# Optimization experiments

Measured on AMD Instinct MI355X. Metric: run time of the kernel, lower is better.

Reference implementation:

```python
import jax, jax.numpy as jnp
import numpy as np

B, N, D, H = 4, 2048, 256, 8
DH = D // H

def setup_inputs() -> dict:
    key = jax.random.key(0)
    ks = jax.random.split(key, 7)
    s = 1.0 / np.sqrt(DH)
    return {
        "sequences": jax.random.normal(ks[0], (B, N, D), dtype=jnp.float32),
        "Wq": jax.random.uniform(ks[1], (H, DH, DH), jnp.float32, -s, s),
        "bq": jax.random.uniform(ks[2], (H, DH), jnp.float32, -s, s),
        "Wk": jax.random.uniform(ks[3], (H, DH, DH), jnp.float32, -s, s),
        "bk": jax.random.uniform(ks[4], (H, DH), jnp.float32, -s, s),
        "Wv": jax.random.uniform(ks[5], (H, DH, DH), jnp.float32, -s, s),
        "bv": jax.random.uniform(ks[6], (H, DH), jnp.float32, -s, s),
    }

def reference(sequences, Wq, bq, Wk, bk, Wv, bv):
    # sequences: [B, N, D] -> [B, N, H, DH] (head h sees columns h*DH:(h+1)*DH)
    x = sequences.reshape(B, N, H, DH)
    # per-head Linear: y = x @ W.T + b
    q = jnp.einsum("bnhd,hed->bnhe", x, Wq) + bq
    k = jnp.einsum("bnhd,hed->bnhe", x, Wk) + bk
    v = jnp.einsum("bnhd,hed->bnhe", x, Wv) + bv
    scores = jnp.einsum("bnhe,bmhe->bhnm", q, k) / jnp.sqrt(jnp.float32(DH))
    attn = jax.nn.softmax(scores, axis=-1)  # [B, H, N, N]
    out = jnp.einsum("bhnm,bmhe->bnhe", attn, v)
    # hstack of per-head results == concat over last dim == reshape
    return out.reshape(B, N, D)
```

## Files before the change

kernel.cpp:

```cpp
#include <hip/hip_runtime.h>
#include <hip/hip_bf16.h>

typedef __bf16 bf16;
typedef __bf16 bf16x8 __attribute__((ext_vector_type(8)));
typedef __bf16 bf16x4 __attribute__((ext_vector_type(4)));
typedef float  f32x4  __attribute__((ext_vector_type(4)));

#define B_  4
#define N_  2048
#define D_  256
#define H_  8
#define DH_ 32
#define QKV_ELEMS (B_*H_*N_*DH_)

#define QSC    (0.17677669529663687f * 1.4426950408889634f)
#define NBIAS  (-17.312340490667562f)

#if __has_builtin(__builtin_amdgcn_exp2f)
__device__ inline float exp2_hw(float x) { return __builtin_amdgcn_exp2f(x); }
#else
__device__ inline float exp2_hw(float x) {
    float r; asm volatile("v_exp_f32 %0, %1" : "=v"(r) : "v"(x)); return r;
}
#endif

__device__ inline bf16x8 ldcvt8(const float* __restrict__ p) {
    f32x4 a = *(const f32x4*)p;
    f32x4 b = *(const f32x4*)(p + 4);
    bf16x8 r;
    r[0] = (bf16)a[0]; r[1] = (bf16)a[1]; r[2] = (bf16)a[2]; r[3] = (bf16)a[3];
    r[4] = (bf16)b[0]; r[5] = (bf16)b[1]; r[6] = (bf16)b[2]; r[7] = (bf16)b[3];
    return r;
}

__global__ __launch_bounds__(256, 4) void qkv_proj_kernel(
    const float* __restrict__ x,
    const float* __restrict__ Wq, const float* __restrict__ bq,
    const float* __restrict__ Wk, const float* __restrict__ bk,
    const float* __restrict__ Wv, const float* __restrict__ bv,
    bf16* __restrict__ Qg, bf16* __restrict__ Kg, bf16* __restrict__ Vg)
{
    const int nt = blockIdx.x & 31, bh = blockIdx.x >> 5;
    const int h  = bh & (H_-1),    b  = bh >> 3;
    const int wave = threadIdx.x >> 6, lane = threadIdx.x & 63;
    const int l16 = lane & 15, q4 = lane >> 4;
    const int n0 = nt*64 + wave*16;

    bf16x8 xf = ldcvt8(x + ((size_t)(b*N_ + n0 + l16))*D_ + h*DH_ + q4*8);
    f32x4 z = {0.f,0.f,0.f,0.f};

    #pragma unroll
    for (int half = 0; half < 2; ++half) {
        {
            bf16x8 wqf = ldcvt8(Wq + (h*DH_ + half*16 + l16)*DH_ + q4*8);
            bf16x8 wkf = ldcvt8(Wk + (h*DH_ + half*16 + l16)*DH_ + q4*8);
            f32x4 dq = __builtin_amdgcn_mfma_f32_16x16x32_bf16(wqf, xf, z, 0, 0, 0);
            f32x4 dk = __builtin_amdgcn_mfma_f32_16x16x32_bf16(wkf, xf, z, 0, 0, 0);
            f32x4 bq4 = *(const f32x4*)(bq + h*DH_ + half*16 + q4*4);
            f32x4 bk4 = *(const f32x4*)(bk + h*DH_ + half*16 + q4*4);
            bf16x4 pq, pk;
            #pragma unroll
            for (int r = 0; r < 4; ++r) {
                pq[r] = (bf16)((dq[r] + bq4[r]) * QSC);
                pk[r] = (bf16)(dk[r] + bk4[r]);
            }
            const size_t row = ((size_t)bh*N_ + n0 + l16)*DH_ + half*16 + q4*4;
            *(bf16x4*)(Qg + row) = pq;
            *(bf16x4*)(Kg + row) = pk;
        }
        {
            bf16x8 wvf = ldcvt8(Wv + (h*DH_ + half*16 + l16)*DH_ + q4*8);
            f32x4 dv = __builtin_amdgcn_mfma_f32_16x16x32_bf16(xf, wvf, z, 0, 0, 0);
            const float bb = bv[h*DH_ + half*16 + l16];
            bf16x4 pv;
            #pragma unroll
            for (int r = 0; r < 4; ++r) pv[r] = (bf16)(dv[r] + bb);
            const int e = half*16 + l16;
            const size_t idx = ((size_t)bh << 16) + ((size_t)(n0 >> 5) << 10)
                             + (e << 5) + (q4 << 3) + (((n0 >> 4) & 1) << 2);
            *(bf16x4*)(Vg + idx) = pv;
        }
    }
}

__global__ __launch_bounds__(256, 2) void attn_kernel(
    const bf16* __restrict__ Qg, const bf16* __restrict__ Kg,
    const bf16* __restrict__ Vg, float* __restrict__ out)
{
    const int qt = blockIdx.x & 15;
    const int bh = blockIdx.x >> 4;
    const int h  = bh & (H_-1), b = bh >> 3;
    const int lane = threadIdx.x & 63;
    const int wave = threadIdx.x >> 6;
    const int l16 = lane & 15, q4 = lane >> 4;

    const bf16* Kb = Kg + (size_t)bh*N_*DH_;
    const bf16* Vb = Vg + ((size_t)bh << 16);
    const int qrow0 = qt*128 + wave*32;

    bf16x8 qb0 = *(const bf16x8*)(Qg + ((size_t)bh*N_ + qrow0 + l16)*DH_ + q4*8);
    bf16x8 qb1 = *(const bf16x8*)(Qg + ((size_t)bh*N_ + qrow0 + 16 + l16)*DH_ + q4*8);

    bf16x8 ones;
    #pragma unroll
    for (int j = 0; j < 8; ++j) ones[j] = (bf16)1.0f;

    f32x4 ot[2][2];
    f32x4 osum[2];
    #pragma unroll
    for (int i = 0; i < 2; ++i) {
        ot[i][0] = (f32x4){0,0,0,0}; ot[i][1] = (f32x4){0,0,0,0};
        osum[i]  = (f32x4){0,0,0,0};
    }

    bf16x8 kf[8], vf[8];
    #pragma unroll
    for (int kc = 0; kc < 8; ++kc)
        kf[kc] = *(const bf16x8*)(Kb + (size_t)(kc*16 + l16)*DH_ + q4*8);
    #pragma unroll
    for (int i = 0; i < 8; ++i)
        vf[i] = *(const bf16x8*)(Vb + (size_t)(i >> 1)*1024 + ((i & 1)*16 + l16)*32 + q4*8);

    const f32x4 zb = {NBIAS, NBIAS, NBIAS, NBIAS};

    for (int kt = 0; kt < 16; ++kt) {
        f32x4 st[8][2];
        #pragma unroll
        for (int kc = 0; kc < 8; ++kc) {
            st[kc][0] = __builtin_amdgcn_mfma_f32_16x16x32_bf16(kf[kc], qb0, zb, 0, 0, 0);
            st[kc][1] = __builtin_amdgcn_mfma_f32_16x16x32_bf16(kf[kc], qb1, zb, 0, 0, 0);
        }

        const int nkt = (kt + 1) & 15;
        const bf16* Kn = Kb + (size_t)nkt*128*DH_;
        #pragma unroll
        for (int kc = 0; kc < 8; ++kc)
            kf[kc] = *(const bf16x8*)(Kn + (size_t)(kc*16 + l16)*DH_ + q4*8);

        bf16x8 pb[4][2];
        #pragma unroll
        for (int kc = 0; kc < 8; ++kc)
            #pragma unroll
            for (int qh = 0; qh < 2; ++qh)
                #pragma unroll
                for (int r = 0; r < 4; ++r)
                    pb[kc >> 1][qh][(kc & 1)*4 + r] = (bf16)exp2_hw(st[kc][qh][r]);

        #pragma unroll
        for (int kk = 0; kk < 4; ++kk) {
            #pragma unroll
            for (int dhh = 0; dhh < 2; ++dhh) {
                ot[dhh][0] = __builtin_amdgcn_mfma_f32_16x16x32_bf16(vf[kk*2 + dhh], pb[kk][0], ot[dhh][0], 0, 0, 0);
                ot[dhh][1] = __builtin_amdgcn_mfma_f32_16x16x32_bf16(vf[kk*2 + dhh], pb[kk][1], ot[dhh][1], 0, 0, 0);
            }
            osum[0] = __builtin_amdgcn_mfma_f32_16x16x32_bf16(ones, pb[kk][0], osum[0], 0, 0, 0);
            osum[1] = __builtin_amdgcn_mfma_f32_16x16x32_bf16(ones, pb[kk][1], osum[1], 0, 0, 0);
        }

        const bf16* Vn = Vb + (size_t)nkt*128*DH_;
        #pragma unroll
        for (int i = 0; i < 8; ++i)
            vf[i] = *(const bf16x8*)(Vn + (size_t)(i >> 1)*1024 + ((i & 1)*16 + l16)*32 + q4*8);
    }

    #pragma unroll
    for (int qh = 0; qh < 2; ++qh) {
        const float inv = 1.0f / osum[qh][0];
        #pragma unroll
        for (int dhh = 0; dhh < 2; ++dhh) {
            f32x4 o;
            #pragma unroll
            for (int r = 0; r < 4; ++r) o[r] = ot[dhh][qh][r] * inv;
            *(f32x4*)(out + ((size_t)b*N_ + qrow0 + qh*16 + l16)*D_
                          + h*DH_ + dhh*16 + q4*4) = o;
        }
    }
}

extern "C" void kernel_launch(void* const* d_in, const int* in_sizes, int n_in,
                              void* d_out, int out_size, void* d_ws, size_t ws_size,
                              hipStream_t stream)
{
    const float* x  = (const float*)d_in[0];
    const float* Wq = (const float*)d_in[1];
    const float* bq = (const float*)d_in[2];
    const float* Wk = (const float*)d_in[3];
    const float* bk = (const float*)d_in[4];
    const float* Wv = (const float*)d_in[5];
    const float* bv = (const float*)d_in[6];
    float* out = (float*)d_out;

    bf16* Qg = (bf16*)d_ws;
    bf16* Kg = Qg + QKV_ELEMS;
    bf16* Vg = Kg + QKV_ELEMS;

    qkv_proj_kernel<<<dim3(B_*H_*(N_/64)), dim3(256), 0, stream>>>(
        x, Wq, bq, Wk, bk, Wv, bv, Qg, Kg, Vg);
    attn_kernel<<<dim3(B_*H_*(N_/128)), dim3(256), 0, stream>>>(Qg, Kg, Vg, out);
}
```

Before: 116.5 us.

## Halve attention query tile per wave and loop projection blocks over four row tiles

The attention kernel now gives each wave 16 query rows instead of 32 and launches twice as many blocks with occupancy hint 4. This lowers register pressure and raises parallelism, but every K/V tile is re-read by twice as many waves. The V fragments are now loaded inside the current iteration instead of prefetched, so load latency may be exposed. The projection kernel loads weights and biases once per block, loops over four 64-row tiles, and uses a quarter of the blocks.

```diff
diff --git a/kernel.cpp b/kernel.cpp
--- a/kernel.cpp
+++ b/kernel.cpp
@@ -40,41 +40,45 @@
     const float* __restrict__ Wv, const float* __restrict__ bv,
     bf16* __restrict__ Qg, bf16* __restrict__ Kg, bf16* __restrict__ Vg)
 {
-    const int nt = blockIdx.x & 31, bh = blockIdx.x >> 5;
-    const int h  = bh & (H_-1),    b  = bh >> 3;
+    const int nt8 = blockIdx.x & 7, bh = blockIdx.x >> 3;
+    const int h   = bh & (H_-1),   b  = bh >> 3;
     const int wave = threadIdx.x >> 6, lane = threadIdx.x & 63;
     const int l16 = lane & 15, q4 = lane >> 4;
-    const int n0 = nt*64 + wave*16;
 
-    bf16x8 xf = ldcvt8(x + ((size_t)(b*N_ + n0 + l16))*D_ + h*DH_ + q4*8);
-    f32x4 z = {0.f,0.f,0.f,0.f};
-
+    bf16x8 wqf[2], wkf[2], wvf[2];
+    f32x4  bq4[2], bk4[2];
+    float  bvs[2];
     #pragma unroll
     for (int half = 0; half < 2; ++half) {
-        {
-            bf16x8 wqf = ldcvt8(Wq + (h*DH_ + half*16 + l16)*DH_ + q4*8);
-            bf16x8 wkf = ldcvt8(Wk + (h*DH_ + half*16 + l16)*DH_ + q4*8);
-            f32x4 dq = __builtin_amdgcn_mfma_f32_16x16x32_bf16(wqf, xf, z, 0, 0, 0);
-            f32x4 dk = __builtin_amdgcn_mfma_f32_16x16x32_bf16(wkf, xf, z, 0, 0, 0);
-            f32x4 bq4 = *(const f32x4*)(bq + h*DH_ + half*16 + q4*4);
-            f32x4 bk4 = *(const f32x4*)(bk + h*DH_ + half*16 + q4*4);
-            bf16x4 pq, pk;
+        wqf[half] = ldcvt8(Wq + (h*DH_ + half*16 + l16)*DH_ + q4*8);
+        wkf[half] = ldcvt8(Wk + (h*DH_ + half*16 + l16)*DH_ + q4*8);
+        wvf[half] = ldcvt8(Wv + (h*DH_ + half*16 + l16)*DH_ + q4*8);
+        bq4[half] = *(const f32x4*)(bq + h*DH_ + half*16 + q4*4);
+        bk4[half] = *(const f32x4*)(bk + h*DH_ + half*16 + q4*4);
+        bvs[half] = bv[h*DH_ + half*16 + l16];
+    }
+
+    const f32x4 z = {0.f,0.f,0.f,0.f};
+    #pragma unroll
+    for (int it = 0; it < 4; ++it) {
+        const int n0 = nt8*256 + it*64 + wave*16;
+        bf16x8 xf = ldcvt8(x + ((size_t)(b*N_ + n0 + l16))*D_ + h*DH_ + q4*8);
+
+        #pragma unroll
+        for (int half = 0; half < 2; ++half) {
+            f32x4 dq = __builtin_amdgcn_mfma_f32_16x16x32_bf16(wqf[half], xf, z, 0, 0, 0);
+            f32x4 dk = __builtin_amdgcn_mfma_f32_16x16x32_bf16(wkf[half], xf, z, 0, 0, 0);
+            f32x4 dv = __builtin_amdgcn_mfma_f32_16x16x32_bf16(xf, wvf[half], z, 0, 0, 0);
+            bf16x4 pq, pk, pv;
             #pragma unroll
             for (int r = 0; r < 4; ++r) {
-                pq[r] = (bf16)((dq[r] + bq4[r]) * QSC);
-                pk[r] = (bf16)(dk[r] + bk4[r]);
+                pq[r] = (bf16)((dq[r] + bq4[half][r]) * QSC);
+                pk[r] = (bf16)(dk[r] + bk4[half][r]);
+                pv[r] = (bf16)(dv[r] + bvs[half]);
             }
             const size_t row = ((size_t)bh*N_ + n0 + l16)*DH_ + half*16 + q4*4;
             *(bf16x4*)(Qg + row) = pq;
             *(bf16x4*)(Kg + row) = pk;
-        }
-        {
-            bf16x8 wvf = ldcvt8(Wv + (h*DH_ + half*16 + l16)*DH_ + q4*8);
-            f32x4 dv = __builtin_amdgcn_mfma_f32_16x16x32_bf16(xf, wvf, z, 0, 0, 0);
-            const float bb = bv[h*DH_ + half*16 + l16];
-            bf16x4 pv;
-            #pragma unroll
-            for (int r = 0; r < 4; ++r) pv[r] = (bf16)(dv[r] + bb);
             const int e = half*16 + l16;
             const size_t idx = ((size_t)bh << 16) + ((size_t)(n0 >> 5) << 10)
                              + (e << 5) + (q4 << 3) + (((n0 >> 4) & 1) << 2);
@@ -83,12 +87,12 @@
     }
 }
 
-__global__ __launch_bounds__(256, 2) void attn_kernel(
+__global__ __launch_bounds__(256, 4) void attn_kernel(
     const bf16* __restrict__ Qg, const bf16* __restrict__ Kg,
     const bf16* __restrict__ Vg, float* __restrict__ out)
 {
-    const int qt = blockIdx.x & 15;
-    const int bh = blockIdx.x >> 4;
+    const int qt = blockIdx.x & 31;
+    const int bh = blockIdx.x >> 5;
     const int h  = bh & (H_-1), b = bh >> 3;
     const int lane = threadIdx.x & 63;
     const int wave = threadIdx.x >> 6;
@@ -96,40 +100,28 @@
 
     const bf16* Kb = Kg + (size_t)bh*N_*DH_;
     const bf16* Vb = Vg + ((size_t)bh << 16);
-    const int qrow0 = qt*128 + wave*32;
+    const int qrow0 = qt*64 + wave*16;
 
-    bf16x8 qb0 = *(const bf16x8*)(Qg + ((size_t)bh*N_ + qrow0 + l16)*DH_ + q4*8);
-    bf16x8 qb1 = *(const bf16x8*)(Qg + ((size_t)bh*N_ + qrow0 + 16 + l16)*DH_ + q4*8);
+    bf16x8 qb = *(const bf16x8*)(Qg + ((size_t)bh*N_ + qrow0 + l16)*DH_ + q4*8);
 
     bf16x8 ones;
     #pragma unroll
     for (int j = 0; j < 8; ++j) ones[j] = (bf16)1.0f;
 
-    f32x4 ot[2][2];
-    f32x4 osum[2];
-    #pragma unroll
-    for (int i = 0; i < 2; ++i) {
-        ot[i][0] = (f32x4){0,0,0,0}; ot[i][1] = (f32x4){0,0,0,0};
-        osum[i]  = (f32x4){0,0,0,0};
-    }
+    f32x4 ot0 = {0,0,0,0}, ot1 = {0,0,0,0}, osum = {0,0,0,0};
 
-    bf16x8 kf[8], vf[8];
+    bf16x8 kf[8];
     #pragma unroll
     for (int kc = 0; kc < 8; ++kc)
         kf[kc] = *(const bf16x8*)(Kb + (size_t)(kc*16 + l16)*DH_ + q4*8);
-    #pragma unroll
-    for (int i = 0; i < 8; ++i)
-        vf[i] = *(const bf16x8*)(Vb + (size_t)(i >> 1)*1024 + ((i & 1)*16 + l16)*32 + q4*8);
 
     const f32x4 zb = {NBIAS, NBIAS, NBIAS, NBIAS};
 
     for (int kt = 0; kt < 16; ++kt) {
-        f32x4 st[8][2];
+        f32x4 st[8];
         #pragma unroll
-        for (int kc = 0; kc < 8; ++kc) {
-            st[kc][0] = __builtin_amdgcn_mfma_f32_16x16x32_bf16(kf[kc], qb0, zb, 0, 0, 0);
-            st[kc][1] = __builtin_amdgcn_mfma_f32_16x16x32_bf16(kf[kc], qb1, zb, 0, 0, 0);
-        }
+        for (int kc = 0; kc < 8; ++kc)
+            st[kc] = __builtin_amdgcn_mfma_f32_16x16x32_bf16(kf[kc], qb, zb, 0, 0, 0);
 
         const int nkt = (kt + 1) & 15;
         const bf16* Kn = Kb + (size_t)nkt*128*DH_;
@@ -137,43 +129,34 @@
         for (int kc = 0; kc < 8; ++kc)
             kf[kc] = *(const bf16x8*)(Kn + (size_t)(kc*16 + l16)*DH_ + q4*8);
 
-        bf16x8 pb[4][2];
+        bf16x8 vf[8];
+        const bf16* Vc = Vb + (size_t)kt*128*DH_;
         #pragma unroll
-        for (int kc = 0; kc < 8; ++kc)
-            #pragma unroll
-            for (int qh = 0; qh < 2; ++qh)
-                #pragma unroll
-                for (int r = 0; r < 4; ++r)
-                    pb[kc >> 1][qh][(kc & 1)*4 + r] = (bf16)exp2_hw(st[kc][qh][r]);
+        for (int i = 0; i < 8; ++i)
+            vf[i] = *(const bf16x8*)(Vc + (size_t)(i >> 1)*1024 + ((i & 1)*16 + l16)*32 + q4*8);
 
         #pragma unroll
         for (int kk = 0; kk < 4; ++kk) {
+            bf16x8 pb;
             #pragma unroll
-            for (int dhh = 0; dhh < 2; ++dhh) {
-                ot[dhh][0] = __builtin_amdgcn_mfma_f32_16x16x32_bf16(vf[kk*2 + dhh], pb[kk][0], ot[dhh][0], 0, 0, 0);
-                ot[dhh][1] = __builtin_amdgcn_mfma_f32_16x16x32_bf16(vf[kk*2 + dhh], pb[kk][1], ot[dhh][1], 0, 0, 0);
-            }
-            osum[0] = __builtin_amdgcn_mfma_f32_16x16x32_bf16(ones, pb[kk][0], osum[0], 0, 0, 0);
-            osum[1] = __builtin_amdgcn_mfma_f32_16x16x32_bf16(ones, pb[kk][1], osum[1], 0, 0, 0);
+            for (int half = 0; half < 2; ++half)
+                #pragma unroll
+                for (int r = 0; r < 4; ++r)
+                    pb[half*4 + r] = (bf16)exp2_hw(st[kk*2 + half][r]);
+            ot0  = __builtin_amdgcn_mfma_f32_16x16x32_bf16(vf[kk*2 + 0], pb, ot0, 0, 0, 0);
+            ot1  = __builtin_amdgcn_mfma_f32_16x16x32_bf16(vf[kk*2 + 1], pb, ot1, 0, 0, 0);
+            osum = __builtin_amdgcn_mfma_f32_16x16x32_bf16(ones, pb, osum, 0, 0, 0);
         }
-
-        const bf16* Vn = Vb + (size_t)nkt*128*DH_;
-        #pragma unroll
-        for (int i = 0; i < 8; ++i)
-            vf[i] = *(const bf16x8*)(Vn + (size_t)(i >> 1)*1024 + ((i & 1)*16 + l16)*32 + q4*8);
     }
 
+    const float inv = 1.0f / osum[0];
     #pragma unroll
-    for (int qh = 0; qh < 2; ++qh) {
-        const float inv = 1.0f / osum[qh][0];
+    for (int dhh = 0; dhh < 2; ++dhh) {
+        const f32x4& o = dhh ? ot1 : ot0;
+        f32x4 w;
         #pragma unroll
-        for (int dhh = 0; dhh < 2; ++dhh) {
-            f32x4 o;
-            #pragma unroll
-            for (int r = 0; r < 4; ++r) o[r] = ot[dhh][qh][r] * inv;
-            *(f32x4*)(out + ((size_t)b*N_ + qrow0 + qh*16 + l16)*D_
-                          + h*DH_ + dhh*16 + q4*4) = o;
-        }
+        for (int r = 0; r < 4; ++r) w[r] = o[r] * inv;
+        *(f32x4*)(out + ((size_t)b*N_ + qrow0 + l16)*D_ + h*DH_ + dhh*16 + q4*4) = w;
     }
 }
 
@@ -194,7 +177,7 @@
     bf16* Kg = Qg + QKV_ELEMS;
     bf16* Vg = Kg + QKV_ELEMS;
 
-    qkv_proj_kernel<<<dim3(B_*H_*(N_/64)), dim3(256), 0, stream>>>(
+    qkv_proj_kernel<<<dim3(B_*H_*8), dim3(256), 0, stream>>>(
         x, Wq, bq, Wk, bk, Wv, bv, Qg, Kg, Vg);
-    attn_kernel<<<dim3(B_*H_*(N_/128)), dim3(256), 0, stream>>>(Qg, Kg, Vg, out);
+    attn_kernel<<<dim3(B_*H_*(N_/64)), dim3(256), 0, stream>>>(Qg, Kg, Vg, out);
 }
```

Result: slower. 133.6 us (+14.7%).
